# Kernel tuning notes

Hardware: AMD Instinct MI355X
Metric: run time of the kernel (lower is better)

Reference implementation:

```python
import jax, jax.numpy as jnp
import numpy as np

B, C, H_IMG, W_IMG = 16, 384, 56, 56
NUM_HEADS = 6
HEAD_DIM = C // NUM_HEADS
BN_EPS = 1e-5


def _bn(x, gamma, beta, mean, var):
    # x: [b, ch, n] or [b, ch, h, w]; per-channel affine normalization (eval-mode BatchNorm)
    shape = (1, -1) + (1,) * (x.ndim - 2)
    scale = (gamma / jnp.sqrt(var + BN_EPS)).reshape(shape)
    shift = (beta - mean * gamma / jnp.sqrt(var + BN_EPS)).reshape(shape)
    return x * scale + shift


def setup_inputs() -> dict:
    key = jax.random.key(0)
    ks = jax.random.split(key, 12)
    c2 = 2 * C
    return {
        "x": jax.random.normal(ks[0], (B, C, H_IMG, W_IMG), jnp.float32),
        "qk_w": jax.random.normal(ks[1], (c2, C // 2), jnp.float32) * 0.05,
        "qk_gamma": jax.random.uniform(ks[2], (c2,), jnp.float32, 0.5, 1.5),
        "qk_beta": jax.random.normal(ks[3], (c2,), jnp.float32) * 0.1,
        "qk_mean": jax.random.normal(ks[4], (c2,), jnp.float32) * 0.1,
        "qk_var": jax.random.uniform(ks[5], (c2,), jnp.float32, 0.5, 1.5),
        "pe_w": jax.random.normal(ks[6], (C, 1, 3, 3), jnp.float32) * 0.1,
        "pe_gamma": jax.random.uniform(ks[7], (C,), jnp.float32, 0.5, 1.5),
        "pe_beta": jax.random.normal(ks[8], (C,), jnp.float32) * 0.1,
        "pe_mean": jax.random.normal(ks[9], (C,), jnp.float32) * 0.1,
        "pe_var": jax.random.uniform(ks[10], (C,), jnp.float32, 0.5, 1.5),
    }


def reference(x, qk_w, qk_gamma, qk_beta, qk_mean, qk_var,
              pe_w, pe_gamma, pe_beta, pe_mean, pe_var):
    b, c, h, w = x.shape
    n = h * w
    s = n ** (-0.5)
    nh, hd = NUM_HEADS, HEAD_DIM

    # grouped (groups=2) 1x1 conv: out channels [0:c] from input [0:c/2], [c:2c] from [c/2:c]
    xg = x.reshape(b, 2, c // 2, n)                       # [b, 2, c/2, n]
    wg = qk_w.reshape(2, c, c // 2)                       # [group, out_per_group, in_per_group]
    qk = jnp.einsum('bgin,goi->bgon', xg, wg).reshape(b, 2 * c, n)
    qk = _bn(qk, qk_gamma, qk_beta, qk_mean, qk_var)
    qk = jax.nn.elu(qk) + 1.0

    qk = qk.reshape(b, 2, nh, hd, n)
    q, k = qk[:, 0], qk[:, 1]                             # [b, H, d, n]
    v = x.reshape(b, nh, hd, n)                           # [b, H, d, n]

    # kv = (k*s) @ (v^T * s): [b, H, d, d]
    kv = jnp.einsum('bhdn,bhen->bhde', k * s, v * s)
    # numerator: q^T @ kv -> [b, H, n, d]
    num = jnp.einsum('bhdn,bhde->bhne', q, kv)
    # denominator: q^T @ mean_n(k) -> [b, H, n]
    den = jnp.einsum('bhdn,bhd->bhn', q, k.mean(axis=-1)) + 1e-6
    attn = (num / den[..., None]).transpose(0, 1, 3, 2).reshape(b, c, h, w)

    # depthwise 3x3 conv positional encoding on v (= x) + BN
    pe = jax.lax.conv_general_dilated(
        x, pe_w, window_strides=(1, 1), padding=((1, 1), (1, 1)),
        feature_group_count=c, dimension_numbers=('NCHW', 'OIHW', 'NCHW'))
    pe = _bn(pe, pe_gamma, pe_beta, pe_mean, pe_var)

    return attn + pe
```

## Files before the change

### kernel.cpp

```cpp
#include <hip/hip_runtime.h>
#include <math.h>

#define N_SP 3136
#define BN_EPS 1e-5f

typedef __attribute__((ext_vector_type(8))) short short8;
typedef __attribute__((ext_vector_type(4))) float f32x4;

#define K_SZ    (16*384*N_SP)
#define KVP_OFF (K_SZ)
#define KVP_SZ  (16*6*7*64*80)
#define KVF_OFF (KVP_OFF + KVP_SZ)
#define KVF_SZ  (16*6*64*64)
#define KM_OFF  (KVF_OFF + KVF_SZ)
#define KM_SZ   (16*6*64)
#define WH_OFF  (KM_OFF + KM_SZ)
#define WSPLIT_N (2*384*192)
#define WF_G    (384*192)
#define PWS_OFF (WH_OFF + WSPLIT_N)
#define PSH_OFF (PWS_OFF + 384*9)
#define QSC_OFF (PSH_OFF + 384)
#define QSH_OFF (QSC_OFF + 384)

#define FSWZ(n) ((((n) >> 1) ^ ((n) >> 2)) & 7)

__device__ __forceinline__ void bsplit(float f, ushort& h, ushort& l) {
    uint u = __float_as_uint(f);
    uint hr = (u + 0x7FFFu + ((u >> 16) & 1u)) >> 16;
    h = (ushort)hr;
    float fh = __uint_as_float(hr << 16);
    float fl = f - fh;
    uint v = __float_as_uint(fl);
    l = (ushort)((v + 0x7FFFu + ((v >> 16) & 1u)) >> 16);
}

__global__ __launch_bounds__(256) void p0_prep(
    const float* __restrict__ qk_w, const float* __restrict__ pe_w,
    const float* __restrict__ qk_gamma, const float* __restrict__ qk_beta,
    const float* __restrict__ qk_mean, const float* __restrict__ qk_var,
    const float* __restrict__ pgamma, const float* __restrict__ pbeta,
    const float* __restrict__ pmean, const float* __restrict__ pvar,
    ushort* __restrict__ wfh, ushort* __restrict__ wfl,
    float* __restrict__ pwsc, float* __restrict__ psh,
    float* __restrict__ qsc, float* __restrict__ qsh)
{
    int idx = blockIdx.x * 256 + threadIdx.x;
    if (idx < WSPLIT_N) {
        int g = (idx >= WF_G) ? 1 : 0;
        int rem = idx - g * WF_G;
        int row = rem / 192, k = rem % 192;
        ushort h, l;
        bsplit(qk_w[idx], h, l);
        int dst = g * WF_G + ((row >> 4) * 24 + (k >> 3)) * 128 + (row & 15) * 8 + (k & 7);
        wfh[dst] = h;
        wfl[dst] = l;
    }
    if (idx < 384) {
        float sc = pgamma[idx] / sqrtf(pvar[idx] + BN_EPS);
        psh[idx] = pbeta[idx] - pmean[idx] * sc;
        #pragma unroll
        for (int q = 0; q < 9; ++q) pwsc[idx * 9 + q] = pe_w[idx * 9 + q] * sc;
        float qs = qk_gamma[idx] / sqrtf(qk_var[idx] + BN_EPS);
        qsc[idx] = qs;
        qsh[idx] = qk_beta[idx] - qk_mean[idx] * qs;
    }
}

__global__ __launch_bounds__(256, 4) void k1_k_mfma(
    const float* __restrict__ x, const ushort* __restrict__ wfh, const ushort* __restrict__ wfl,
    const float* __restrict__ gamma, const float* __restrict__ beta,
    const float* __restrict__ mean, const float* __restrict__ var,
    uint* __restrict__ kq)
{
    __shared__ __align__(16) ushort Bh[4096];
    __shared__ __align__(16) ushort Bl[4096];
    __shared__ float scs[192], shs[192];

    const int bx = blockIdx.x;
    const int by = blockIdx.y;
    const int b = blockIdx.z;
    const int t = threadIdx.x;
    const int lane = t & 63, wv = t >> 6;
    const int lg = lane >> 4, l15 = lane & 15;

    f32x4 acc[3][4];
    #pragma unroll
    for (int mf = 0; mf < 3; ++mf)
        #pragma unroll
        for (int nf = 0; nf < 4; ++nf)
            acc[mf][nf] = (f32x4){0.f, 0.f, 0.f, 0.f};

    const float* xg = x + (size_t)(b * 384 + 192) * N_SP + bx * 64;
    const ushort* wfbh = wfh + WF_G;
    const ushort* wfbl = wfl + WF_G;

    for (int i = t; i < 192; i += 256) {
        int ch = 384 + by * 192 + i;
        float sc = gamma[ch] / sqrtf(var[ch] + BN_EPS);
        scs[i] = sc;
        shs[i] = beta[ch] - mean[ch] * sc;
    }

    for (int kt = 0; kt < 3; ++kt) {
        #pragma unroll
        for (int li = 0; li < 2; ++li) {
            int idx = li * 256 + t;
            int kp = idx >> 4;
            int nq = idx & 15;
            int k0 = kp * 2;
            const float* px = xg + (size_t)(kt * 64 + k0) * N_SP + nq * 4;
            float4 v0 = *(const float4*)px;
            float4 v1 = *(const float4*)(px + N_SP);
            ushort h0[4], l0[4], h1[4], l1[4];
            float a0[4] = {v0.x, v0.y, v0.z, v0.w};
            float a1[4] = {v1.x, v1.y, v1.z, v1.w};
            #pragma unroll
            for (int i2 = 0; i2 < 4; ++i2) { bsplit(a0[i2], h0[i2], l0[i2]); bsplit(a1[i2], h1[i2], l1[i2]); }
            int kb = k0 >> 3, ks = kp & 3;
            #pragma unroll
            for (int i2 = 0; i2 < 4; ++i2) {
                int n = nq * 4 + i2;
                int chunk = n * 8 + (kb ^ FSWZ(n));
                ((uint*)Bh)[chunk * 4 + ks] = (uint)h0[i2] | ((uint)h1[i2] << 16);
                ((uint*)Bl)[chunk * 4 + ks] = (uint)l0[i2] | ((uint)l1[i2] << 16);
            }
        }
        __syncthreads();
        #pragma unroll
        for (int s = 0; s < 2; ++s) {
            int kbq = s * 4 + lg;
            int kglob = kt * 8 + kbq;
            short8 bh[4], bl[4];
            #pragma unroll
            for (int nf = 0; nf < 4; ++nf) {
                int n = nf * 16 + l15;
                int chunk = n * 8 + (kbq ^ FSWZ(n));
                bh[nf] = *(const short8*)&Bh[chunk * 8];
                bl[nf] = *(const short8*)&Bl[chunk * 8];
            }
            #pragma unroll
            for (int mf = 0; mf < 3; ++mf) {
                int rb = by * 12 + wv * 3 + mf;
                int off = (rb * 24 + kglob) * 128 + l15 * 8;
                short8 ah = *(const short8*)&wfbh[off];
                short8 al = *(const short8*)&wfbl[off];
                #pragma unroll
                for (int nf = 0; nf < 4; ++nf) {
                    acc[mf][nf] = __builtin_amdgcn_mfma_f32_16x16x32_bf16(ah, bh[nf], acc[mf][nf], 0, 0, 0);
                    acc[mf][nf] = __builtin_amdgcn_mfma_f32_16x16x32_bf16(ah, bl[nf], acc[mf][nf], 0, 0, 0);
                    acc[mf][nf] = __builtin_amdgcn_mfma_f32_16x16x32_bf16(al, bh[nf], acc[mf][nf], 0, 0, 0);
                }
            }
        }
        __syncthreads();
    }

    size_t obase = ((size_t)b * 384 + by * 192) * N_SP + bx * 64;
    #pragma unroll
    for (int mf = 0; mf < 3; ++mf)
        #pragma unroll
        for (int nf = 0; nf < 4; ++nf) {
            #pragma unroll
            for (int r = 0; r < 4; ++r) {
                int lrow = wv * 48 + mf * 16 + lg * 4 + r;
                float v = acc[mf][nf][r] * scs[lrow] + shs[lrow];
                v = v > 0.f ? v + 1.f : __expf(v);
                ushort hh, ll;
                bsplit(v, hh, ll);
                kq[obase + (size_t)lrow * N_SP + nf * 16 + l15] = (uint)hh | ((uint)ll << 16);
            }
        }
}

__global__ __launch_bounds__(256) void k2_kv_mfma(
    const float* __restrict__ x, const uint* __restrict__ kq,
    float* __restrict__ kv_part)
{
    __shared__ __align__(16) ushort Kh[4096], Kl[4096];
    __shared__ __align__(16) ushort Vh[5120], Vl[5120];

    const int chunk = blockIdx.x;
    const int h = blockIdx.y, b = blockIdx.z;
    const int t = threadIdx.x;
    const int lane = t & 63, wv = t >> 6;
    const int lg = lane >> 4, l15 = lane & 15;

    const uint* kp  = kq + (size_t)(b*384 + h*64) * N_SP;
    const float* vp = x  + (size_t)(b*384 + h*64) * N_SP;

    #pragma unroll
    for (int li = 0; li < 4; ++li) {
        int idx = li * 256 + t;
        int row = 64 + (idx >> 6), col = idx & 63;
        int off = (row * 8 + ((col >> 3) ^ (row & 7))) * 8 + (col & 7);
        Vh[off] = (row == 64) ? (ushort)0x3F80 : (ushort)0;
        Vl[off] = 0;
    }

    f32x4 acc[5];
    #pragma unroll
    for (int nf = 0; nf < 5; ++nf) acc[nf] = (f32x4){0.f, 0.f, 0.f, 0.f};

    for (int sub = 0; sub < 7; ++sub) {
        int n0 = chunk * 448 + sub * 64;
        #pragma unroll
        for (int li = 0; li < 4; ++li) {
            int idx = li * 256 + t;
            int row = idx >> 4, sc = idx & 15;
            int off = (row * 8 + ((sc >> 1) ^ (row & 7))) * 8 + (sc & 1) * 4;
            uint4 kf = *(const uint4*)&kp[(size_t)row * N_SP + n0 + sc * 4];
            ((uint*)&Kh[off])[0] = (kf.x & 0xFFFFu) | (kf.y << 16);
            ((uint*)&Kh[off])[1] = (kf.z & 0xFFFFu) | (kf.w << 16);
            ((uint*)&Kl[off])[0] = (kf.x >> 16) | (kf.y & 0xFFFF0000u);
            ((uint*)&Kl[off])[1] = (kf.z >> 16) | (kf.w & 0xFFFF0000u);
            float4 vf = *(const float4*)&vp[(size_t)row * N_SP + n0 + sc * 4];
            ushort h0,h1,h2,h3,l0,l1,l2,l3;
            bsplit(vf.x,h0,l0); bsplit(vf.y,h1,l1); bsplit(vf.z,h2,l2); bsplit(vf.w,h3,l3);
            ((uint*)&Vh[off])[0] = (uint)h0 | ((uint)h1 << 16);
            ((uint*)&Vh[off])[1] = (uint)h2 | ((uint)h3 << 16);
            ((uint*)&Vl[off])[0] = (uint)l0 | ((uint)l1 << 16);
            ((uint*)&Vl[off])[1] = (uint)l2 | ((uint)l3 << 16);
        }
        __syncthreads();
        #pragma unroll
        for (int s = 0; s < 2; ++s) {
            int arow = wv * 16 + l15;
            int akb = (s * 4 + lg) ^ (arow & 7);
            short8 ah = *(const short8*)&Kh[(arow * 8 + akb) * 8];
            short8 al = *(const short8*)&Kl[(arow * 8 + akb) * 8];
            #pragma unroll
            for (int nf = 0; nf < 5; ++nf) {
                int brow = nf * 16 + l15;
                int bkb = (s * 4 + lg) ^ (brow & 7);
                short8 bh = *(const short8*)&Vh[(brow * 8 + bkb) * 8];
                short8 bl = *(const short8*)&Vl[(brow * 8 + bkb) * 8];
                acc[nf] = __builtin_amdgcn_mfma_f32_16x16x32_bf16(ah, bh, acc[nf], 0, 0, 0);
                acc[nf] = __builtin_amdgcn_mfma_f32_16x16x32_bf16(ah, bl, acc[nf], 0, 0, 0);
                acc[nf] = __builtin_amdgcn_mfma_f32_16x16x32_bf16(al, bh, acc[nf], 0, 0, 0);
            }
        }
        __syncthreads();
    }

    size_t base = (size_t)((b*6 + h)*7 + chunk) * 64 * 80;
    #pragma unroll
    for (int nf = 0; nf < 5; ++nf)
        #pragma unroll
        for (int r = 0; r < 4; ++r) {
            int d = wv * 16 + lg * 4 + r;
            kv_part[base + (size_t)d * 80 + nf * 16 + l15] = acc[nf][r];
        }
}

__global__ __launch_bounds__(256) void k2b_reduce(
    const float* __restrict__ kv_part,
    float* __restrict__ kvf, float* __restrict__ km)
{
    const int bh = blockIdx.x;
    const int t = threadIdx.x;
    const float inv_n = 1.0f / (float)N_SP;
    const float* base = kv_part + (size_t)bh * 7 * 5120;
    float s[20];
    #pragma unroll
    for (int j = 0; j < 20; ++j) s[j] = 0.f;
    for (int c = 0; c < 7; ++c) {
        #pragma unroll
        for (int j = 0; j < 20; ++j) s[j] += base[c * 5120 + j * 256 + t];
    }
    #pragma unroll
    for (int j = 0; j < 20; ++j) {
        int i = j * 256 + t;
        int d = i / 80, e = i % 80;
        float v = s[j] * inv_n;
        if (e < 64)       kvf[(size_t)bh * 4096 + d * 64 + e] = v;
        else if (e == 64) km[bh * 64 + d] = v;
    }
}

__global__ __launch_bounds__(256) void k3_attn_pe(
    const float* __restrict__ x,
    const ushort* __restrict__ wfh, const ushort* __restrict__ wfl,
    const float* __restrict__ qsc, const float* __restrict__ qsh,
    const float* __restrict__ kvf, const float* __restrict__ km,
    const float* __restrict__ pwsc, const float* __restrict__ psh,
    float* __restrict__ out)
{
    __shared__ float qs[64][68];
    __shared__ float kms[64];
    ushort* Bh = (ushort*)&qs[0][0];
    ushort* Bl = Bh + 4096;

    const int bx = blockIdx.x;
    const int h = blockIdx.y, b = blockIdx.z;
    const int t = threadIdx.x;
    const int lane = t & 63, wv = t >> 6;
    const int lg = lane >> 4, l15 = lane & 15;
    const int n0 = bx * 64;

    const float* xg = x + (size_t)b * 384 * N_SP + n0;
    const ushort* wfbh = wfh;
    const ushort* wfbl = wfl;

    f32x4 qacc[4];
    #pragma unroll
    for (int nf = 0; nf < 4; ++nf) qacc[nf] = (f32x4){0.f, 0.f, 0.f, 0.f};

    for (int kt = 0; kt < 3; ++kt) {
        #pragma unroll
        for (int li = 0; li < 2; ++li) {
            int idx = li * 256 + t;
            int kp = idx >> 4;
            int nq = idx & 15;
            int k0 = kp * 2;
            const float* px = xg + (size_t)(kt * 64 + k0) * N_SP + nq * 4;
            float4 v0 = *(const float4*)px;
            float4 v1 = *(const float4*)(px + N_SP);
            ushort h0[4], l0[4], h1[4], l1[4];
            float a0[4] = {v0.x, v0.y, v0.z, v0.w};
            float a1[4] = {v1.x, v1.y, v1.z, v1.w};
            #pragma unroll
            for (int i = 0; i < 4; ++i) { bsplit(a0[i], h0[i], l0[i]); bsplit(a1[i], h1[i], l1[i]); }
            int kb = k0 >> 3, ks = kp & 3;
            #pragma unroll
            for (int i = 0; i < 4; ++i) {
                int n = nq * 4 + i;
                int chunk = n * 8 + (kb ^ FSWZ(n));
                ((uint*)Bh)[chunk * 4 + ks] = (uint)h0[i] | ((uint)h1[i] << 16);
                ((uint*)Bl)[chunk * 4 + ks] = (uint)l0[i] | ((uint)l1[i] << 16);
            }
        }
        __syncthreads();
        #pragma unroll
        for (int s = 0; s < 2; ++s) {
            int kbq = s * 4 + lg;
            int kglob = kt * 8 + kbq;
            short8 bh[4], bl[4];
            #pragma unroll
            for (int nf = 0; nf < 4; ++nf) {
                int n = nf * 16 + l15;
                int chunk = n * 8 + (kbq ^ FSWZ(n));
                bh[nf] = *(const short8*)&Bh[chunk * 8];
                bl[nf] = *(const short8*)&Bl[chunk * 8];
            }
            int rb = h * 4 + wv;
            int off = (rb * 24 + kglob) * 128 + l15 * 8;
            short8 ah = *(const short8*)&wfbh[off];
            short8 al = *(const short8*)&wfbl[off];
            #pragma unroll
            for (int nf = 0; nf < 4; ++nf) {
                qacc[nf] = __builtin_amdgcn_mfma_f32_16x16x32_bf16(ah, bh[nf], qacc[nf], 0, 0, 0);
                qacc[nf] = __builtin_amdgcn_mfma_f32_16x16x32_bf16(ah, bl[nf], qacc[nf], 0, 0, 0);
                qacc[nf] = __builtin_amdgcn_mfma_f32_16x16x32_bf16(al, bh[nf], qacc[nf], 0, 0, 0);
            }
        }
        __syncthreads();
    }

    {
        float sc4[4], sh4[4];
        #pragma unroll
        for (int r = 0; r < 4; ++r) {
            int ch = h * 64 + wv * 16 + lg * 4 + r;
            sc4[r] = qsc[ch];
            sh4[r] = qsh[ch];
        }
        #pragma unroll
        for (int nf = 0; nf < 4; ++nf) {
            int col = nf * 16 + l15;
            #pragma unroll
            for (int r = 0; r < 4; ++r) {
                int row = wv * 16 + lg * 4 + r;
                float v = qacc[nf][r] * sc4[r] + sh4[r];
                v = v > 0.f ? v + 1.f : __expf(v);
                qs[row][col] = v;
            }
        }
    }
    if (t < 64) kms[t] = km[(b * 6 + h) * 64 + t];
    __syncthreads();

    const int tx = t & 15, ty = t >> 4;
    const float* kvp = kvf + (size_t)(b * 6 + h) * 4096;
    float acc[4][4] = {};
    float den[4] = {};
    #pragma unroll 8
    for (int d = 0; d < 64; ++d) {
        float4 qn = *(const float4*)&qs[d][tx * 4];
        float4 ke = *(const float4*)&kvp[d * 64 + ty * 4];
        float qq[4] = {qn.x, qn.y, qn.z, qn.w}, kk[4] = {ke.x, ke.y, ke.z, ke.w};
        float kmd = kms[d];
        #pragma unroll
        for (int p = 0; p < 4; ++p) {
            den[p] += qq[p] * kmd;
            #pragma unroll
            for (int j = 0; j < 4; ++j) acc[p][j] += qq[p] * kk[j];
        }
    }

    const int p0 = n0 + tx * 4;
    const int y = p0 / 56, xc = p0 % 56;
    #pragma unroll
    for (int j = 0; j < 4; ++j) {
        int c = h * 64 + ty * 4 + j;
        const float* xp = x + ((size_t)b * 384 + c) * N_SP;
        float s6[3][6];
        #pragma unroll
        for (int dy = 0; dy < 3; ++dy) {
            int yy = y + dy - 1;
            bool yok = (yy >= 0) && (yy < 56);
            float4 mid = make_float4(0.f, 0.f, 0.f, 0.f);
            float lf = 0.f, rt = 0.f;
            if (yok) {
                const float* xr = xp + yy * 56;
                mid = *(const float4*)&xr[xc];
                if (xc > 0)  lf = xr[xc - 1];
                if (xc < 52) rt = xr[xc + 4];
            }
            s6[dy][0] = lf;  s6[dy][1] = mid.x; s6[dy][2] = mid.y;
            s6[dy][3] = mid.z; s6[dy][4] = mid.w; s6[dy][5] = rt;
        }
        float w9[9];
        #pragma unroll
        for (int q = 0; q < 9; ++q) w9[q] = pwsc[c * 9 + q];
        float sh2 = psh[c];
        float4 r;
        float* pr = (float*)&r;
        #pragma unroll
        for (int p = 0; p < 4; ++p) {
            float conv = 0.f;
            #pragma unroll
            for (int dy = 0; dy < 3; ++dy)
                #pragma unroll
                for (int dx = 0; dx < 3; ++dx)
                    conv += w9[dy * 3 + dx] * s6[dy][p + dx];
            pr[p] = acc[p][j] / (den[p] + 1e-6f) + conv + sh2;
        }
        *(float4*)&out[((size_t)b * 384 + c) * N_SP + p0] = r;
    }
}

extern "C" void kernel_launch(void* const* d_in, const int* in_sizes, int n_in,
                              void* d_out, int out_size, void* d_ws, size_t ws_size,
                              hipStream_t stream)
{
    const float* x        = (const float*)d_in[0];
    const float* qk_w     = (const float*)d_in[1];
    const float* qk_gamma = (const float*)d_in[2];
    const float* qk_beta  = (const float*)d_in[3];
    const float* qk_mean  = (const float*)d_in[4];
    const float* qk_var   = (const float*)d_in[5];
    const float* pe_w     = (const float*)d_in[6];
    const float* pe_gamma = (const float*)d_in[7];
    const float* pe_beta  = (const float*)d_in[8];
    const float* pe_mean  = (const float*)d_in[9];
    const float* pe_var   = (const float*)d_in[10];
    float* out = (float*)d_out;

    float* ws      = (float*)d_ws;
    uint* kq       = (uint*)ws;
    float* kv_part = ws + KVP_OFF;
    float* kvf     = ws + KVF_OFF;
    float* km      = ws + KM_OFF;
    ushort* wfh    = (ushort*)(ws + WH_OFF);
    ushort* wfl    = wfh + WSPLIT_N;
    float* pwsc    = ws + PWS_OFF;
    float* psh     = ws + PSH_OFF;
    float* qsc     = ws + QSC_OFF;
    float* qsh     = ws + QSH_OFF;

    hipLaunchKernelGGL(p0_prep, dim3((WSPLIT_N + 255)/256), dim3(256), 0, stream,
                       qk_w, pe_w, qk_gamma, qk_beta, qk_mean, qk_var,
                       pe_gamma, pe_beta, pe_mean, pe_var,
                       wfh, wfl, pwsc, psh, qsc, qsh);
    dim3 g1(49, 2, 16);
    hipLaunchKernelGGL(k1_k_mfma, g1, dim3(256), 0, stream,
                       x, wfh, wfl, qk_gamma, qk_beta, qk_mean, qk_var, kq);
    dim3 g2(7, 6, 16);
    hipLaunchKernelGGL(k2_kv_mfma, g2, dim3(256), 0, stream, x, kq, kv_part);
    hipLaunchKernelGGL(k2b_reduce, dim3(96), dim3(256), 0, stream,
                       kv_part, kvf, km);
    dim3 g3(49, 6, 16);
    hipLaunchKernelGGL(k3_attn_pe, g3, dim3(256), 0, stream,
                       x, wfh, wfl, qsc, qsh, kvf, km, pwsc, psh, out);
}
```

Measured before the change: 208.2 us.

## Compute attention numerator and denominator in k3 with split-bf16 MFMA

The scalar FMA loop that multiplied q by kv and k-mean in k3 is replaced by MFMA instructions using a three-product hi/lo bf16 split. The reduce kernel now writes kv and k-mean transposed as hi/lo bf16 pairs, with k-mean folded in as an extra row. q is stored to shared memory as bf16 fragments, and the results are staged back through shared memory for the epilogue. Launch bounds are raised to request 4 blocks per CU. The aim is to offload the per-tile 64x64x64 product onto matrix cores, at the cost of extra shared-memory round trips, syncs and a small precision loss from the split-bf16 approximation.

```diff
diff --git a/kernel.cpp b/kernel.cpp
--- a/kernel.cpp
+++ b/kernel.cpp
@@ -10,11 +10,9 @@
 #define K_SZ    (16*384*N_SP)
 #define KVP_OFF (K_SZ)
 #define KVP_SZ  (16*6*7*64*80)
-#define KVF_OFF (KVP_OFF + KVP_SZ)
-#define KVF_SZ  (16*6*64*64)
-#define KM_OFF  (KVF_OFF + KVF_SZ)
-#define KM_SZ   (16*6*64)
-#define WH_OFF  (KM_OFF + KM_SZ)
+#define KVT_OFF (KVP_OFF + KVP_SZ)
+#define KVT_FSZ (2*96*80*64/2)
+#define WH_OFF  (KVT_OFF + KVT_FSZ)
 #define WSPLIT_N (2*384*192)
 #define WF_G    (384*192)
 #define PWS_OFF (WH_OFF + WSPLIT_N)
@@ -254,12 +252,14 @@
 
 __global__ __launch_bounds__(256) void k2b_reduce(
     const float* __restrict__ kv_part,
-    float* __restrict__ kvf, float* __restrict__ km)
+    ushort* __restrict__ kvt_h, ushort* __restrict__ kvt_l)
 {
     const int bh = blockIdx.x;
     const int t = threadIdx.x;
     const float inv_n = 1.0f / (float)N_SP;
     const float* base = kv_part + (size_t)bh * 7 * 5120;
+    ushort* oh = kvt_h + (size_t)bh * 5120;
+    ushort* ol = kvt_l + (size_t)bh * 5120;
     float s[20];
     #pragma unroll
     for (int j = 0; j < 20; ++j) s[j] = 0.f;
@@ -271,23 +271,24 @@
     for (int j = 0; j < 20; ++j) {
         int i = j * 256 + t;
         int d = i / 80, e = i % 80;
-        float v = s[j] * inv_n;
-        if (e < 64)       kvf[(size_t)bh * 4096 + d * 64 + e] = v;
-        else if (e == 64) km[bh * 64 + d] = v;
-    }
-}
-
-__global__ __launch_bounds__(256) void k3_attn_pe(
+        ushort h, l;
+        bsplit(s[j] * inv_n, h, l);
+        oh[e * 64 + d] = h;
+        ol[e * 64 + d] = l;
+    }
+}
+
+#define ATT_STRIDE 68
+__global__ __launch_bounds__(256, 4) void k3_attn_pe(
     const float* __restrict__ x,
     const ushort* __restrict__ wfh, const ushort* __restrict__ wfl,
     const float* __restrict__ qsc, const float* __restrict__ qsh,
-    const float* __restrict__ kvf, const float* __restrict__ km,
+    const ushort* __restrict__ kvt_h, const ushort* __restrict__ kvt_l,
     const float* __restrict__ pwsc, const float* __restrict__ psh,
     float* __restrict__ out)
 {
-    __shared__ float qs[64][68];
-    __shared__ float kms[64];
-    ushort* Bh = (ushort*)&qs[0][0];
+    __shared__ __align__(16) float SBF[ATT_STRIDE * 64 + 64];
+    ushort* Bh = (ushort*)&SBF[0];
     ushort* Bl = Bh + 4096;
 
     const int bx = blockIdx.x;
@@ -298,8 +299,6 @@
     const int n0 = bx * 64;
 
     const float* xg = x + (size_t)b * 384 * N_SP + n0;
-    const ushort* wfbh = wfh;
-    const ushort* wfbl = wfl;
 
     f32x4 qacc[4];
     #pragma unroll
@@ -344,8 +343,8 @@
             }
             int rb = h * 4 + wv;
             int off = (rb * 24 + kglob) * 128 + l15 * 8;
-            short8 ah = *(const short8*)&wfbh[off];
-            short8 al = *(const short8*)&wfbl[off];
+            short8 ah = *(const short8*)&wfh[off];
+            short8 al = *(const short8*)&wfl[off];
             #pragma unroll
             for (int nf = 0; nf < 4; ++nf) {
                 qacc[nf] = __builtin_amdgcn_mfma_f32_16x16x32_bf16(ah, bh[nf], qacc[nf], 0, 0, 0);
@@ -364,41 +363,80 @@
             sc4[r] = qsc[ch];
             sh4[r] = qsh[ch];
         }
+        int hc = wv * 4 + lg;
         #pragma unroll
         for (int nf = 0; nf < 4; ++nf) {
-            int col = nf * 16 + l15;
+            ushort hh[4], ll[4];
             #pragma unroll
             for (int r = 0; r < 4; ++r) {
-                int row = wv * 16 + lg * 4 + r;
                 float v = qacc[nf][r] * sc4[r] + sh4[r];
                 v = v > 0.f ? v + 1.f : __expf(v);
-                qs[row][col] = v;
-            }
-        }
-    }
-    if (t < 64) kms[t] = km[(b * 6 + h) * 64 + t];
+                bsplit(v, hh[r], ll[r]);
+            }
+            int n = nf * 16 + l15;
+            uint2 uh, ul;
+            uh.x = (uint)hh[0] | ((uint)hh[1] << 16);
+            uh.y = (uint)hh[2] | ((uint)hh[3] << 16);
+            ul.x = (uint)ll[0] | ((uint)ll[1] << 16);
+            ul.y = (uint)ll[2] | ((uint)ll[3] << 16);
+            *(uint2*)(Bh + hc * 256 + n * 4) = uh;
+            *(uint2*)(Bl + hc * 256 + n * 4) = ul;
+        }
+    }
     __syncthreads();
 
+    short8 bqh[2], bql[2];
+    #pragma unroll
+    for (int s = 0; s < 2; ++s) {
+        int hc = (s * 4 + lg) * 2;
+        const ushort* ph = Bh + hc * 256 + (wv * 16 + l15) * 4;
+        uint2 a0 = *(const uint2*)ph;
+        uint2 a1 = *(const uint2*)(ph + 256);
+        uint* pp = (uint*)&bqh[s];
+        pp[0] = a0.x; pp[1] = a0.y; pp[2] = a1.x; pp[3] = a1.y;
+        const ushort* pl = Bl + hc * 256 + (wv * 16 + l15) * 4;
+        uint2 c0 = *(const uint2*)pl;
+        uint2 c1 = *(const uint2*)(pl + 256);
+        uint* qq = (uint*)&bql[s];
+        qq[0] = c0.x; qq[1] = c0.y; qq[2] = c1.x; qq[3] = c1.y;
+    }
+    __syncthreads();
+
+    const ushort* ahb = kvt_h + (size_t)(b * 6 + h) * 5120;
+    const ushort* alb = kvt_l + (size_t)(b * 6 + h) * 5120;
+    f32x4 pacc[5];
+    #pragma unroll
+    for (int m = 0; m < 5; ++m) pacc[m] = (f32x4){0.f, 0.f, 0.f, 0.f};
+    #pragma unroll
+    for (int s = 0; s < 2; ++s) {
+        #pragma unroll
+        for (int m = 0; m < 5; ++m) {
+            int off = (m * 16 + l15) * 64 + (s * 4 + lg) * 8;
+            short8 ah = *(const short8*)&ahb[off];
+            short8 al = *(const short8*)&alb[off];
+            pacc[m] = __builtin_amdgcn_mfma_f32_16x16x32_bf16(ah, bqh[s], pacc[m], 0, 0, 0);
+            pacc[m] = __builtin_amdgcn_mfma_f32_16x16x32_bf16(ah, bql[s], pacc[m], 0, 0, 0);
+            pacc[m] = __builtin_amdgcn_mfma_f32_16x16x32_bf16(al, bqh[s], pacc[m], 0, 0, 0);
+        }
+    }
+    {
+        int ncol = wv * 16 + l15;
+        #pragma unroll
+        for (int m = 0; m < 4; ++m)
+            #pragma unroll
+            for (int r = 0; r < 4; ++r)
+                SBF[(m * 16 + lg * 4 + r) * ATT_STRIDE + ncol] = pacc[m][r];
+        if (lg == 0)
+            SBF[ATT_STRIDE * 64 + ncol] = pacc[4][0];
+    }
+    __syncthreads();
+
     const int tx = t & 15, ty = t >> 4;
-    const float* kvp = kvf + (size_t)(b * 6 + h) * 4096;
-    float acc[4][4] = {};
-    float den[4] = {};
-    #pragma unroll 8
-    for (int d = 0; d < 64; ++d) {
-        float4 qn = *(const float4*)&qs[d][tx * 4];
-        float4 ke = *(const float4*)&kvp[d * 64 + ty * 4];
-        float qq[4] = {qn.x, qn.y, qn.z, qn.w}, kk[4] = {ke.x, ke.y, ke.z, ke.w};
-        float kmd = kms[d];
-        #pragma unroll
-        for (int p = 0; p < 4; ++p) {
-            den[p] += qq[p] * kmd;
-            #pragma unroll
-            for (int j = 0; j < 4; ++j) acc[p][j] += qq[p] * kk[j];
-        }
-    }
-
     const int p0 = n0 + tx * 4;
     const int y = p0 / 56, xc = p0 % 56;
+    float den[4];
+    #pragma unroll
+    for (int p = 0; p < 4; ++p) den[p] = SBF[ATT_STRIDE * 64 + tx * 4 + p] + 1e-6f;
     #pragma unroll
     for (int j = 0; j < 4; ++j) {
         int c = h * 64 + ty * 4 + j;
@@ -433,7 +471,7 @@
                 #pragma unroll
                 for (int dx = 0; dx < 3; ++dx)
                     conv += w9[dy * 3 + dx] * s6[dy][p + dx];
-            pr[p] = acc[p][j] / (den[p] + 1e-6f) + conv + sh2;
+            pr[p] = SBF[(ty * 4 + j) * ATT_STRIDE + tx * 4 + p] / den[p] + conv + sh2;
         }
         *(float4*)&out[((size_t)b * 384 + c) * N_SP + p0] = r;
     }
@@ -459,8 +497,8 @@
     float* ws      = (float*)d_ws;
     uint* kq       = (uint*)ws;
     float* kv_part = ws + KVP_OFF;
-    float* kvf     = ws + KVF_OFF;
-    float* km      = ws + KM_OFF;
+    ushort* kvt_h  = (ushort*)(ws + KVT_OFF);
+    ushort* kvt_l  = kvt_h + 96 * 5120;
     ushort* wfh    = (ushort*)(ws + WH_OFF);
     ushort* wfl    = wfh + WSPLIT_N;
     float* pwsc    = ws + PWS_OFF;
@@ -478,8 +516,8 @@
     dim3 g2(7, 6, 16);
     hipLaunchKernelGGL(k2_kv_mfma, g2, dim3(256), 0, stream, x, kq, kv_part);
     hipLaunchKernelGGL(k2b_reduce, dim3(96), dim3(256), 0, stream,
-                       kv_part, kvf, km);
+                       kv_part, kvt_h, kvt_l);
     dim3 g3(49, 6, 16);
     hipLaunchKernelGGL(k3_attn_pe, g3, dim3(256), 0, stream,
-                       x, wfh, wfl, qsc, qsh, kvf, km, pwsc, psh, out);
-}
+                       x, wfh, wfl, qsc, qsh, kvt_h, kvt_l, pwsc, psh, out);
+}
```

Measured after the change: 209.7 us. About the same (+0.7%).
